# Kernel optimization log

Measured on AMD Instinct MI355X. Metric: run time of the kernel, lower is better.

The kernel has to match this reference:

```python
import jax, jax.numpy as jnp
import numpy as np

ALPHA = 0.2  # leaky-relu slope (relu_a)
EPS = 1e-16  # guard for isolated nodes (matches pyGAT div-by-rowsum semantics up to eps)


def sp_gat_layer(x, row, col, W, a1, a2, concat):
    # pyGAT sparse attention layer (eval mode, no dropout).
    N = x.shape[0]
    h = x @ W                                   # [N, F_out]
    # a @ [h_src || h_dst] decomposed to avoid materializing edge_h [E, 2F]
    logits = h[row] @ a1 + h[col] @ a2          # [E]
    e = jnp.exp(-jax.nn.leaky_relu(logits, ALPHA))
    rowsum = jax.ops.segment_sum(e, row, num_segments=N)                 # [N]
    hp = jax.ops.segment_sum(e[:, None] * h[col], row, num_segments=N)  # [N, F_out]
    hp = hp / (rowsum[:, None] + EPS)
    return jax.nn.elu(hp) if concat else hp


def setup_inputs() -> dict:
    key = jax.random.key(0)
    ks = jax.random.split(key, 12)
    N, E = 50000, 800000
    nfeat, nhid, nclass, nstruc, nheads = 256, 32, 40, 128, 8
    hid = nhid * nheads  # 256

    def xav(k, shape):
        fan = shape[-2] + shape[-1]
        return jax.random.uniform(k, shape, jnp.float32, -1.0, 1.0) * jnp.sqrt(6.0 / fan)

    x = jax.random.normal(ks[0], (N, nfeat), jnp.float32)
    edge_index = jax.random.randint(ks[1], (2, E), 0, N, jnp.int32)
    W_att = xav(ks[2], (nheads, nfeat, nhid))
    a1 = jax.random.normal(ks[3], (nheads, nhid), jnp.float32) * 0.1
    a2 = jax.random.normal(ks[4], (nheads, nhid), jnp.float32) * 0.1
    W_out = xav(ks[5], (hid, nclass))
    a1_out = jax.random.normal(ks[6], (nclass,), jnp.float32) * 0.1
    a2_out = jax.random.normal(ks[7], (nclass,), jnp.float32) * 0.1
    W_gc = xav(ks[8], (hid, hid))
    b_gc = jnp.zeros((hid,), jnp.float32)
    W_enc = xav(ks[9], (hid, nstruc))
    b_enc = jnp.zeros((nstruc,), jnp.float32)
    return dict(x=x, edge_index=edge_index, W_att=W_att, a1=a1, a2=a2,
                W_out=W_out, a1_out=a1_out, a2_out=a2_out,
                W_gc=W_gc, b_gc=b_gc, W_enc=W_enc, b_enc=b_enc)


def reference(x, edge_index, W_att, a1, a2, W_out, a1_out, a2_out, W_gc, b_gc, W_enc, b_enc):
    N = x.shape[0]
    row, col = edge_index[0], edge_index[1]
    nheads = W_att.shape[0]
    # multi-head sparse attention, concat (loop over fixed small head count)
    heads = [sp_gat_layer(x, row, col, W_att[i], a1[i], a2[i], True) for i in range(nheads)]
    h1 = jnp.concatenate(heads, axis=1)                 # [N, nhid*nheads]
    # GraphConvolution: adj @ (h1 @ W) + b  (binary adjacency from edge list)
    support = h1 @ W_gc                                 # [N, hid]
    h2 = jax.ops.segment_sum(support[col], row, num_segments=N) + b_gc
    # output attention head (concat=False) then elu
    xo = jax.nn.elu(sp_gat_layer(h2, row, col, W_out, a1_out, a2_out, False))
    y = h1 @ W_enc + b_enc
    z = h2 @ W_enc + b_enc
    return (jax.nn.log_softmax(xo, axis=1), y, z)
```

## Files before the change

### kernel.cpp

```cpp
#include <hip/hip_runtime.h>
#include <math.h>

typedef __attribute__((ext_vector_type(8))) short short8;
typedef __attribute__((ext_vector_type(4))) ushort u16x4;
typedef __attribute__((ext_vector_type(8))) ushort u16x8;
typedef __attribute__((ext_vector_type(8))) __bf16 bf16x8;
typedef __attribute__((ext_vector_type(4))) float f32x4;

__device__ inline ushort f2bf(float x) {
  union { float f; unsigned u; } v; v.f = x;
  unsigned r = v.u + 0x7fff + ((v.u >> 16) & 1);
  return (ushort)(r >> 16);
}
__device__ inline float bf2f(ushort b) {
  union { unsigned u; float f; } v; v.u = (unsigned)b << 16; return v.f;
}

template <int F, int Fp>
__global__ void pack_b(const float* __restrict__ B, ushort* __restrict__ Bp) {
  int tid = blockIdx.x * blockDim.x + threadIdx.x;
  if (tid >= 256 * Fp) return;
  int k = tid / Fp, n = tid % Fp;
  float val = (n < F) ? B[k * F + n] : 0.f;
  int kb = k >> 5, kr = k & 31;
  int lane = ((kr >> 3) << 4) | (n & 15);
  int j = kr & 7;
  int nb = n >> 4;
  size_t off = ((size_t)(kb * (Fp / 16) + nb) * 64 + lane) * 8 + j;
  Bp[off] = f2bf(val);
}

__global__ void pack_watt_frag(const float* __restrict__ W_att, ushort* __restrict__ Bp) {
  int tid = blockIdx.x * blockDim.x + threadIdx.x;
  if (tid >= 256 * 256) return;
  int k = tid >> 8, n = tid & 255;
  float val = W_att[(size_t)(n >> 5) * 8192 + k * 32 + (n & 31)];
  int kb = k >> 5, kr = k & 31;
  int lane = ((kr >> 3) << 4) | (n & 15);
  int j = kr & 7;
  int nb = n >> 4;
  size_t off = ((size_t)(kb * 16 + nb) * 64 + lane) * 8 + j;
  Bp[off] = f2bf(val);
}

template <int Fp, int F, int OUTMODE, bool BIAS, bool BFIN>
__global__ __launch_bounds__(512) void gemm_mfma(const float* __restrict__ A,
                                                 const ushort* __restrict__ Ab,
                                                 const ushort* __restrict__ Bp,
                                                 const float* __restrict__ bias,
                                                 float* __restrict__ C,
                                                 ushort* __restrict__ Cb, int N) {
  constexpr int NB = Fp / 64;
  __shared__ ushort lhs[32 * 256];
  int n0 = blockIdx.x * 32;
  int t = threadIdx.x;
  {
    int r = t >> 4, q = t & 15;
    int row = n0 + r;
    bool rin = row < N;
#pragma unroll
    for (int i = 0; i < 2; ++i) {
      int c0 = q * 16 + i * 8;
      int c8 = (c0 >> 3) ^ (r & 7);
      if (BFIN) {
        u16x8 hv = (u16x8){0, 0, 0, 0, 0, 0, 0, 0};
        if (rin) hv = *reinterpret_cast<const u16x8*>(Ab + (size_t)row * 256 + c0);
        *reinterpret_cast<u16x8*>(&lhs[r * 256 + c8 * 8]) = hv;
      } else {
        float4 f0 = {0.f, 0.f, 0.f, 0.f}, f1 = {0.f, 0.f, 0.f, 0.f};
        if (rin) {
          f0 = *reinterpret_cast<const float4*>(A + (size_t)row * 256 + c0);
          f1 = *reinterpret_cast<const float4*>(A + (size_t)row * 256 + c0 + 4);
        }
        float ff[8] = {f0.x, f0.y, f0.z, f0.w, f1.x, f1.y, f1.z, f1.w};
        short8 sh;
#pragma unroll
        for (int j = 0; j < 8; ++j) sh[j] = (short)f2bf(ff[j]);
        *reinterpret_cast<short8*>(&lhs[r * 256 + c8 * 8]) = sh;
      }
    }
  }
  __syncthreads();
  int w = t >> 6, l = t & 63;
  int wr = w >> 2, wc = w & 3;
  int lr = l & 15, lk = l >> 4;
  f32x4 acc[NB];
#pragma unroll
  for (int nb = 0; nb < NB; ++nb) acc[nb] = (f32x4){0.f, 0.f, 0.f, 0.f};

#pragma unroll
  for (int ks = 0; ks < 8; ++ks) {
    int row = wr * 16 + lr;
    int c8 = (ks * 4 + lk) ^ (row & 7);
    bf16x8 ah = *reinterpret_cast<const bf16x8*>(&lhs[row * 256 + c8 * 8]);
#pragma unroll
    for (int nb = 0; nb < NB; ++nb) {
      size_t off = ((size_t)(ks * (Fp / 16) + wc * NB + nb) * 64 + l) * 8;
      bf16x8 bh = *reinterpret_cast<const bf16x8*>(&Bp[off]);
      acc[nb] = __builtin_amdgcn_mfma_f32_16x16x32_bf16(ah, bh, acc[nb], 0, 0, 0);
    }
  }
  int rowbase = n0 + wr * 16 + lk * 4;
#pragma unroll
  for (int nb = 0; nb < NB; ++nb) {
    int col = wc * (NB * 16) + nb * 16 + lr;
    if (col < F) {
      float bi = BIAS ? bias[col] : 0.f;
#pragma unroll
      for (int rg = 0; rg < 4; ++rg) {
        if (rowbase + rg < N) {
          float v = acc[nb][rg] + bi;
          if (OUTMODE != 2) C[(size_t)(rowbase + rg) * F + col] = v;
          if (OUTMODE != 0) Cb[(size_t)(rowbase + rg) * F + col] = f2bf(v);
        }
      }
    }
  }
}

__global__ void calc_s12(const ushort* __restrict__ Hb, const float* __restrict__ a1,
                         const float* __restrict__ a2, float* __restrict__ s1,
                         float* __restrict__ s2, int N) {
  int tid = blockIdx.x * blockDim.x + threadIdx.x;
  if (tid >= N * 8) return;
  int h = tid & 7;
  int n = tid >> 3;
  const ushort* hp = Hb + (size_t)n * 256 + h * 32;
  const float* A1 = a1 + h * 32;
  const float* A2 = a2 + h * 32;
  float d1 = 0.f, d2 = 0.f;
#pragma unroll
  for (int j0 = 0; j0 < 32; j0 += 8) {
    u16x8 hv = *reinterpret_cast<const u16x8*>(hp + j0);
#pragma unroll
    for (int j = 0; j < 8; ++j) {
      float v = bf2f(hv[j]);
      d1 = fmaf(v, A1[j0 + j], d1);
      d2 = fmaf(v, A2[j0 + j], d2);
    }
  }
  s1[tid] = d1;
  s2[tid] = d2;
}

__global__ void calc_s12_out(const float* __restrict__ Ho, const float* __restrict__ a1o,
                             const float* __restrict__ a2o, float* __restrict__ s1o,
                             float* __restrict__ s2o, int N) {
  int n = blockIdx.x * blockDim.x + threadIdx.x;
  if (n >= N) return;
  const float* hp = Ho + (size_t)n * 40;
  float d1 = 0.f, d2 = 0.f;
#pragma unroll
  for (int j = 0; j < 40; ++j) {
    float v = hp[j];
    d1 = fmaf(v, a1o[j], d1);
    d2 = fmaf(v, a2o[j], d2);
  }
  s1o[n] = d1;
  s2o[n] = d2;
}

__global__ void hist_deg(const int* __restrict__ row, int* __restrict__ deg, int E) {
  int e = blockIdx.x * blockDim.x + threadIdx.x;
  if (e < E) atomicAdd(&deg[row[e]], 1);
}

__global__ void scan1(const int* __restrict__ deg, int* __restrict__ rp, int* __restrict__ bsum,
                      int N) {
  __shared__ int sd[256];
  int t = threadIdx.x;
  int i = blockIdx.x * 256 + t;
  int v = (i < N) ? deg[i] : 0;
  sd[t] = v;
  __syncthreads();
  for (int off = 1; off < 256; off <<= 1) {
    int x = (t >= off) ? sd[t - off] : 0;
    __syncthreads();
    sd[t] += x;
    __syncthreads();
  }
  if (i < N) rp[i] = sd[t] - v;
  if (t == 255) bsum[blockIdx.x] = sd[255];
}

__global__ void scan2(int* __restrict__ bsum, int nb) {
  __shared__ int sd[256];
  int t = threadIdx.x;
  int v = (t < nb) ? bsum[t] : 0;
  sd[t] = v;
  __syncthreads();
  for (int off = 1; off < 256; off <<= 1) {
    int x = (t >= off) ? sd[t - off] : 0;
    __syncthreads();
    sd[t] += x;
    __syncthreads();
  }
  if (t < nb) bsum[t] = sd[t] - v;
}

__global__ void scan3(int* __restrict__ rp, const int* __restrict__ bsum, int N, int E) {
  int i = blockIdx.x * 256 + threadIdx.x;
  if (i < N) rp[i] += bsum[blockIdx.x];
  if (i == 0) rp[N] = E;
}

__global__ void scatter_edges(const int* __restrict__ row, const int* __restrict__ col,
                              const int* __restrict__ rp, int* __restrict__ cur,
                              int* __restrict__ scol, int* __restrict__ srow, int E) {
  int e = blockIdx.x * blockDim.x + threadIdx.x;
  if (e >= E) return;
  int r = row[e];
  int p = atomicAdd(&cur[r], 1);
  int idx = rp[r] + p;
  scol[idx] = col[e];
  srow[idx] = r;
}

__global__ void edge_wo(const int* __restrict__ srow, const int* __restrict__ scol,
                        const float* __restrict__ s1o, const float* __restrict__ s2o,
                        float* __restrict__ wo, int E) {
  int e = blockIdx.x * blockDim.x + threadIdx.x;
  if (e >= E) return;
  float lg = s1o[srow[e]] + s2o[scol[e]];
  float lr = lg > 0.f ? lg : 0.2f * lg;
  wo[e] = expf(-lr);
}

__global__ __launch_bounds__(64) void agg_att(const ushort* __restrict__ Hb,
                                              const float* __restrict__ s1,
                                              const float* __restrict__ s2,
                                              const int* __restrict__ rp,
                                              const int* __restrict__ scol,
                                              ushort* __restrict__ h1b, int N) {
  int n = blockIdx.x;
  int t = threadIdx.x;
  int head = t >> 3;
  float s1n = s1[n * 8 + head];
  float acc[4] = {0.f, 0.f, 0.f, 0.f};
  float rs = 0.f;
  int beg = rp[n], end = rp[n + 1];
  for (int i = beg; i < end; ++i) {
    int c = scol[i];
    float lg = s1n + s2[c * 8 + head];
    float lr = lg > 0.f ? lg : 0.2f * lg;
    float wv = expf(-lr);
    rs += wv;
    const u16x4 hv = *reinterpret_cast<const u16x4*>(Hb + (size_t)c * 256 + t * 4);
#pragma unroll
    for (int j = 0; j < 4; ++j) acc[j] = fmaf(wv, bf2f(hv[j]), acc[j]);
  }
  float inv = 1.f / (rs + 1e-16f);
  u16x4 ov;
#pragma unroll
  for (int j = 0; j < 4; ++j) {
    float v = acc[j] * inv;
    v = v > 0.f ? v : expm1f(v);
    ov[j] = f2bf(v);
  }
  *reinterpret_cast<u16x4*>(h1b + (size_t)n * 256 + t * 4) = ov;
}

__global__ __launch_bounds__(64) void agg_gc(const ushort* __restrict__ Sb,
                                             const int* __restrict__ rp,
                                             const int* __restrict__ scol,
                                             const float* __restrict__ b_gc,
                                             ushort* __restrict__ h2b, int N) {
  int n = blockIdx.x;
  int t = threadIdx.x;
  float acc[4] = {0.f, 0.f, 0.f, 0.f};
  int beg = rp[n], end = rp[n + 1];
  for (int i = beg; i < end; ++i) {
    int c = scol[i];
    const u16x4 sv = *reinterpret_cast<const u16x4*>(Sb + (size_t)c * 256 + t * 4);
#pragma unroll
    for (int j = 0; j < 4; ++j) acc[j] += bf2f(sv[j]);
  }
  const float4 bv = *reinterpret_cast<const float4*>(b_gc + t * 4);
  float o[4] = {acc[0] + bv.x, acc[1] + bv.y, acc[2] + bv.z, acc[3] + bv.w};
  u16x4 ov;
#pragma unroll
  for (int j = 0; j < 4; ++j) ov[j] = f2bf(o[j]);
  *reinterpret_cast<u16x4*>(h2b + (size_t)n * 256 + t * 4) = ov;
}

__global__ __launch_bounds__(64) void agg_out_lsm(const ushort* __restrict__ Hob,
                                                  const float* __restrict__ wo,
                                                  const int* __restrict__ rp,
                                                  const int* __restrict__ scol,
                                                  float* __restrict__ out0, int N) {
  int n = blockIdx.x;
  int t = threadIdx.x;
  float acc = 0.f, rs = 0.f;
  int beg = rp[n], end = rp[n + 1];
  for (int i = beg; i < end; ++i) {
    int c = scol[i];
    float wv = wo[i];
    rs += wv;
    if (t < 40) acc = fmaf(wv, bf2f(Hob[(size_t)c * 40 + t]), acc);
  }
  float hp = acc / (rs + 1e-16f);
  float xo = (t < 40) ? (hp > 0.f ? hp : expm1f(hp)) : -3.0e38f;
  float mx = xo;
#pragma unroll
  for (int m = 1; m < 64; m <<= 1) mx = fmaxf(mx, __shfl_xor(mx, m));
  float ex = (t < 40) ? expf(xo - mx) : 0.f;
  float sum = ex;
#pragma unroll
  for (int m = 1; m < 64; m <<= 1) sum += __shfl_xor(sum, m);
  if (t < 40) out0[(size_t)n * 40 + t] = xo - mx - logf(sum);
}

extern "C" void kernel_launch(void* const* d_in, const int* in_sizes, int n_in,
                              void* d_out, int out_size, void* d_ws, size_t ws_size,
                              hipStream_t stream) {
  const float* x      = (const float*)d_in[0];
  const int*   ei     = (const int*)d_in[1];
  const float* W_att  = (const float*)d_in[2];
  const float* a1     = (const float*)d_in[3];
  const float* a2     = (const float*)d_in[4];
  const float* W_out  = (const float*)d_in[5];
  const float* a1_out = (const float*)d_in[6];
  const float* a2_out = (const float*)d_in[7];
  const float* W_gc   = (const float*)d_in[8];
  const float* b_gc   = (const float*)d_in[9];
  const float* W_enc  = (const float*)d_in[10];
  const float* b_enc  = (const float*)d_in[11];

  const int N = in_sizes[0] / 256;
  const int E = in_sizes[1] / 2;
  const int* row = ei;
  const int* col = ei + E;

  char* p = (char*)d_ws;
  auto alloc = [&](size_t bytes) -> void* {
    void* r = (void*)p;
    p += (bytes + 255) & ~(size_t)255;
    return r;
  };
  ushort* hbuf = (ushort*)alloc((size_t)N * 256 * 2);
  ushort* h1b  = (ushort*)alloc((size_t)N * 256 * 2);
  ushort* h2b  = (ushort*)alloc((size_t)N * 256 * 2);
  float* Ho   = (float*)alloc((size_t)N * 40 * 4);
  ushort* Hob = (ushort*)alloc((size_t)N * 40 * 2);
  float* s1   = (float*)alloc((size_t)N * 8 * 4);
  float* s2   = (float*)alloc((size_t)N * 8 * 4);
  float* s1o  = (float*)alloc((size_t)N * 4);
  float* s2o  = (float*)alloc((size_t)N * 4);
  int* deg    = (int*)alloc((size_t)N * 4);
  int* rp     = (int*)alloc((size_t)(N + 1) * 4);
  int* bsum   = (int*)alloc(256 * 4);
  int* scol   = (int*)alloc((size_t)E * 4);
  int* srow   = (int*)alloc((size_t)E * 4);
  float* wo   = (float*)alloc((size_t)E * 4);
  ushort* Bp  = (ushort*)alloc((size_t)65536 * 2);
  ushort* Wg  = (ushort*)alloc((size_t)65536 * 2);
  ushort* We  = (ushort*)alloc((size_t)32768 * 2);
  ushort* Wo  = (ushort*)alloc((size_t)16384 * 2);

  float* out0 = (float*)d_out;
  float* outY = out0 + (size_t)N * 40;
  float* outZ = outY + (size_t)N * 128;

  const int nb = (N + 255) / 256;
  const int gblk = (N + 31) / 32;

  pack_watt_frag<<<dim3(256), dim3(256), 0, stream>>>(W_att, Bp);
  pack_b<256, 256><<<dim3(256), dim3(256), 0, stream>>>(W_gc, Wg);
  pack_b<128, 128><<<dim3(128), dim3(256), 0, stream>>>(W_enc, We);
  pack_b<40, 64><<<dim3(64), dim3(256), 0, stream>>>(W_out, Wo);

  hipMemsetAsync(deg, 0, (size_t)N * 4, stream);
  hist_deg<<<dim3((E + 255) / 256), dim3(256), 0, stream>>>(row, deg, E);
  scan1<<<dim3(nb), dim3(256), 0, stream>>>(deg, rp, bsum, N);
  scan2<<<dim3(1), dim3(256), 0, stream>>>(bsum, nb);
  scan3<<<dim3(nb), dim3(256), 0, stream>>>(rp, bsum, N, E);
  hipMemsetAsync(deg, 0, (size_t)N * 4, stream);
  scatter_edges<<<dim3((E + 255) / 256), dim3(256), 0, stream>>>(row, col, rp, deg, scol, srow, E);

  gemm_mfma<256, 256, 2, false, false><<<dim3(gblk), dim3(512), 0, stream>>>(
      x, nullptr, Bp, nullptr, nullptr, hbuf, N);
  calc_s12<<<dim3((N * 8 + 255) / 256), dim3(256), 0, stream>>>(hbuf, a1, a2, s1, s2, N);
  agg_att<<<dim3(N), dim3(64), 0, stream>>>(hbuf, s1, s2, rp, scol, h1b, N);

  gemm_mfma<256, 256, 2, false, true><<<dim3(gblk), dim3(512), 0, stream>>>(
      nullptr, h1b, Wg, nullptr, nullptr, hbuf, N);
  agg_gc<<<dim3(N), dim3(64), 0, stream>>>(hbuf, rp, scol, b_gc, h2b, N);

  gemm_mfma<64, 40, 1, false, true><<<dim3(gblk), dim3(512), 0, stream>>>(
      nullptr, h2b, Wo, nullptr, Ho, Hob, N);
  calc_s12_out<<<dim3((N + 255) / 256), dim3(256), 0, stream>>>(Ho, a1_out, a2_out, s1o, s2o, N);
  edge_wo<<<dim3((E + 255) / 256), dim3(256), 0, stream>>>(srow, scol, s1o, s2o, wo, E);
  agg_out_lsm<<<dim3(N), dim3(64), 0, stream>>>(Hob, wo, rp, scol, out0, N);

  gemm_mfma<128, 128, 0, true, true><<<dim3(gblk), dim3(512), 0, stream>>>(
      nullptr, h1b, We, b_enc, outY, nullptr, N);
  gemm_mfma<128, 128, 0, true, true><<<dim3(gblk), dim3(512), 0, stream>>>(
      nullptr, h2b, We, b_enc, outZ, nullptr, N);
}
```

Measured before the change: 413.1 us.

## Double GEMM row tile, merge weight packing kernels, batch encoder GEMMs

Each GEMM block now handles 64 rows instead of 32, and every wave computes two 16-row MFMA tiles per B fragment. This reuses each global B load twice and halves the number of blocks. The four weight-packing kernels become one launch. h1b and h2b are laid out back to back so the two encoder GEMMs (y and z) run as a single launch over 2N rows, which relies on outY and outZ being contiguous. The larger tile doubles LDS use (32 KB per block) and the per-wave accumulator registers, which may reduce occupancy.

```diff
diff --git a/kernel.cpp b/kernel.cpp
--- a/kernel.cpp
+++ b/kernel.cpp
@@ -16,31 +16,38 @@
   union { unsigned u; float f; } v; v.u = (unsigned)b << 16; return v.f;
 }
 
-template <int F, int Fp>
-__global__ void pack_b(const float* __restrict__ B, ushort* __restrict__ Bp) {
-  int tid = blockIdx.x * blockDim.x + threadIdx.x;
-  if (tid >= 256 * Fp) return;
-  int k = tid / Fp, n = tid % Fp;
-  float val = (n < F) ? B[k * F + n] : 0.f;
+__device__ inline void pack_one(float val, int k, int n, int Fp, ushort* __restrict__ dst) {
   int kb = k >> 5, kr = k & 31;
   int lane = ((kr >> 3) << 4) | (n & 15);
   int j = kr & 7;
   int nb = n >> 4;
   size_t off = ((size_t)(kb * (Fp / 16) + nb) * 64 + lane) * 8 + j;
-  Bp[off] = f2bf(val);
-}
-
-__global__ void pack_watt_frag(const float* __restrict__ W_att, ushort* __restrict__ Bp) {
+  dst[off] = f2bf(val);
+}
+
+__global__ void pack_all(const float* __restrict__ W_att, const float* __restrict__ W_gc,
+                         const float* __restrict__ W_enc, const float* __restrict__ W_out,
+                         ushort* __restrict__ Bp, ushort* __restrict__ Wg,
+                         ushort* __restrict__ We, ushort* __restrict__ Wo) {
   int tid = blockIdx.x * blockDim.x + threadIdx.x;
-  if (tid >= 256 * 256) return;
-  int k = tid >> 8, n = tid & 255;
-  float val = W_att[(size_t)(n >> 5) * 8192 + k * 32 + (n & 31)];
-  int kb = k >> 5, kr = k & 31;
-  int lane = ((kr >> 3) << 4) | (n & 15);
-  int j = kr & 7;
-  int nb = n >> 4;
-  size_t off = ((size_t)(kb * 16 + nb) * 64 + lane) * 8 + j;
-  Bp[off] = f2bf(val);
+  if (tid < 65536) {
+    int k = tid >> 8, n = tid & 255;
+    float val = W_att[(size_t)(n >> 5) * 8192 + k * 32 + (n & 31)];
+    pack_one(val, k, n, 256, Bp);
+  } else if (tid < 131072) {
+    int t2 = tid - 65536;
+    int k = t2 >> 8, n = t2 & 255;
+    pack_one(W_gc[k * 256 + n], k, n, 256, Wg);
+  } else if (tid < 163840) {
+    int t2 = tid - 131072;
+    int k = t2 >> 7, n = t2 & 127;
+    pack_one(W_enc[k * 128 + n], k, n, 128, We);
+  } else if (tid < 180224) {
+    int t2 = tid - 163840;
+    int k = t2 >> 6, n = t2 & 63;
+    float val = (n < 40) ? W_out[k * 40 + n] : 0.f;
+    pack_one(val, k, n, 64, Wo);
+  }
 }
 
 template <int Fp, int F, int OUTMODE, bool BIAS, bool BFIN>
@@ -51,16 +58,16 @@
                                                  float* __restrict__ C,
                                                  ushort* __restrict__ Cb, int N) {
   constexpr int NB = Fp / 64;
-  __shared__ ushort lhs[32 * 256];
-  int n0 = blockIdx.x * 32;
+  __shared__ ushort lhs[64 * 256];
+  int n0 = blockIdx.x * 64;
   int t = threadIdx.x;
   {
-    int r = t >> 4, q = t & 15;
+    int r = t >> 3, q = t & 7;
     int row = n0 + r;
     bool rin = row < N;
 #pragma unroll
-    for (int i = 0; i < 2; ++i) {
-      int c0 = q * 16 + i * 8;
+    for (int i = 0; i < 4; ++i) {
+      int c0 = q * 32 + i * 8;
       int c8 = (c0 >> 3) ^ (r & 7);
       if (BFIN) {
         u16x8 hv = (u16x8){0, 0, 0, 0, 0, 0, 0, 0};
@@ -84,34 +91,45 @@
   int w = t >> 6, l = t & 63;
   int wr = w >> 2, wc = w & 3;
   int lr = l & 15, lk = l >> 4;
-  f32x4 acc[NB];
-#pragma unroll
-  for (int nb = 0; nb < NB; ++nb) acc[nb] = (f32x4){0.f, 0.f, 0.f, 0.f};
+  f32x4 acc[2][NB];
+#pragma unroll
+  for (int m = 0; m < 2; ++m)
+#pragma unroll
+    for (int nb = 0; nb < NB; ++nb) acc[m][nb] = (f32x4){0.f, 0.f, 0.f, 0.f};
 
 #pragma unroll
   for (int ks = 0; ks < 8; ++ks) {
-    int row = wr * 16 + lr;
-    int c8 = (ks * 4 + lk) ^ (row & 7);
-    bf16x8 ah = *reinterpret_cast<const bf16x8*>(&lhs[row * 256 + c8 * 8]);
+    bf16x8 ah[2];
+#pragma unroll
+    for (int m = 0; m < 2; ++m) {
+      int row = wr * 32 + m * 16 + lr;
+      int c8 = (ks * 4 + lk) ^ (row & 7);
+      ah[m] = *reinterpret_cast<const bf16x8*>(&lhs[row * 256 + c8 * 8]);
+    }
 #pragma unroll
     for (int nb = 0; nb < NB; ++nb) {
       size_t off = ((size_t)(ks * (Fp / 16) + wc * NB + nb) * 64 + l) * 8;
       bf16x8 bh = *reinterpret_cast<const bf16x8*>(&Bp[off]);
-      acc[nb] = __builtin_amdgcn_mfma_f32_16x16x32_bf16(ah, bh, acc[nb], 0, 0, 0);
+#pragma unroll
+      for (int m = 0; m < 2; ++m)
+        acc[m][nb] = __builtin_amdgcn_mfma_f32_16x16x32_bf16(ah[m], bh, acc[m][nb], 0, 0, 0);
     }
   }
-  int rowbase = n0 + wr * 16 + lk * 4;
-#pragma unroll
-  for (int nb = 0; nb < NB; ++nb) {
-    int col = wc * (NB * 16) + nb * 16 + lr;
-    if (col < F) {
-      float bi = BIAS ? bias[col] : 0.f;
-#pragma unroll
-      for (int rg = 0; rg < 4; ++rg) {
-        if (rowbase + rg < N) {
-          float v = acc[nb][rg] + bi;
-          if (OUTMODE != 2) C[(size_t)(rowbase + rg) * F + col] = v;
-          if (OUTMODE != 0) Cb[(size_t)(rowbase + rg) * F + col] = f2bf(v);
+#pragma unroll
+  for (int m = 0; m < 2; ++m) {
+    int rowbase = n0 + wr * 32 + m * 16 + lk * 4;
+#pragma unroll
+    for (int nb = 0; nb < NB; ++nb) {
+      int col = wc * (NB * 16) + nb * 16 + lr;
+      if (col < F) {
+        float bi = BIAS ? bias[col] : 0.f;
+#pragma unroll
+        for (int rg = 0; rg < 4; ++rg) {
+          if (rowbase + rg < N) {
+            float v = acc[m][nb][rg] + bi;
+            if (OUTMODE != 2) C[(size_t)(rowbase + rg) * F + col] = v;
+            if (OUTMODE != 0) Cb[(size_t)(rowbase + rg) * F + col] = f2bf(v);
+          }
         }
       }
     }
@@ -338,8 +356,8 @@
     return r;
   };
   ushort* hbuf = (ushort*)alloc((size_t)N * 256 * 2);
-  ushort* h1b  = (ushort*)alloc((size_t)N * 256 * 2);
-  ushort* h2b  = (ushort*)alloc((size_t)N * 256 * 2);
+  ushort* h1b  = (ushort*)alloc((size_t)N * 256 * 2 * 2);
+  ushort* h2b  = h1b + (size_t)N * 256;
   float* Ho   = (float*)alloc((size_t)N * 40 * 4);
   ushort* Hob = (ushort*)alloc((size_t)N * 40 * 2);
   float* s1   = (float*)alloc((size_t)N * 8 * 4);
@@ -359,15 +377,13 @@
 
   float* out0 = (float*)d_out;
   float* outY = out0 + (size_t)N * 40;
-  float* outZ = outY + (size_t)N * 128;
 
   const int nb = (N + 255) / 256;
-  const int gblk = (N + 31) / 32;
-
-  pack_watt_frag<<<dim3(256), dim3(256), 0, stream>>>(W_att, Bp);
-  pack_b<256, 256><<<dim3(256), dim3(256), 0, stream>>>(W_gc, Wg);
-  pack_b<128, 128><<<dim3(128), dim3(256), 0, stream>>>(W_enc, We);
-  pack_b<40, 64><<<dim3(64), dim3(256), 0, stream>>>(W_out, Wo);
+  const int gblk = (N + 63) / 64;
+  const int gblk2 = (2 * N + 63) / 64;
+
+  pack_all<<<dim3((180224 + 255) / 256), dim3(256), 0, stream>>>(
+      W_att, W_gc, W_enc, W_out, Bp, Wg, We, Wo);
 
   hipMemsetAsync(deg, 0, (size_t)N * 4, stream);
   hist_deg<<<dim3((E + 255) / 256), dim3(256), 0, stream>>>(row, deg, E);
@@ -392,8 +408,6 @@
   edge_wo<<<dim3((E + 255) / 256), dim3(256), 0, stream>>>(srow, scol, s1o, s2o, wo, E);
   agg_out_lsm<<<dim3(N), dim3(64), 0, stream>>>(Hob, wo, rp, scol, out0, N);
 
-  gemm_mfma<128, 128, 0, true, true><<<dim3(gblk), dim3(512), 0, stream>>>(
-      nullptr, h1b, We, b_enc, outY, nullptr, N);
-  gemm_mfma<128, 128, 0, true, true><<<dim3(gblk), dim3(512), 0, stream>>>(
-      nullptr, h2b, We, b_enc, outZ, nullptr, N);
-}
+  gemm_mfma<128, 128, 0, true, true><<<dim3(gblk2), dim3(512), 0, stream>>>(
+      nullptr, h1b, We, b_enc, outY, nullptr, 2 * N);
+}
```

After: 405.3 us. About the same (-1.9%).
